# Kernel tuning notes

Measured on AMD Instinct MI355X. Metric: run time of the kernel, lower is better.

## Reference

```python
import jax, jax.numpy as jnp
import numpy as np

D_MODEL = 2048
NUM_HEADS = 16
HEAD_DIM = 128
BATCH = 4
SEQ = 2048


def setup_inputs() -> dict:
    key = jax.random.key(0)
    ks = jax.random.split(key, 5)
    s = 0.02
    return {
        "x": jax.random.normal(ks[0], (BATCH, SEQ, D_MODEL), dtype=jnp.float32),
        "Wq": jax.random.normal(ks[1], (NUM_HEADS * HEAD_DIM, D_MODEL), dtype=jnp.float32) * s,
        "Wk": jax.random.normal(ks[2], (NUM_HEADS * HEAD_DIM, D_MODEL), dtype=jnp.float32) * s,
        "Wv": jax.random.normal(ks[3], (NUM_HEADS * HEAD_DIM, D_MODEL), dtype=jnp.float32) * s,
        "Wo": jax.random.normal(ks[4], (D_MODEL, NUM_HEADS * HEAD_DIM), dtype=jnp.float32) * s,
    }


def _split_heads(t):
    b, s, _ = t.shape
    return t.reshape(b, s, NUM_HEADS, HEAD_DIM).transpose(0, 2, 1, 3)  # [b,h,s,d]


def reference(x, Wq, Wk, Wv, Wo):
    # prefill: QKV proj + causal SDPA + output proj. torch Linear: x @ W.T
    q = _split_heads(x @ Wq.T)
    k = _split_heads(x @ Wk.T)
    v = _split_heads(x @ Wv.T)
    scale = 1.0 / jnp.sqrt(jnp.asarray(HEAD_DIM, dtype=x.dtype))
    scores = jnp.einsum("bhqd,bhkd->bhqk", q, k) * scale
    causal = jnp.tril(jnp.ones((SEQ, SEQ), dtype=bool))
    scores = jnp.where(causal, scores, jnp.finfo(scores.dtype).min)
    attn = jax.nn.softmax(scores, axis=-1)
    y = jnp.einsum("bhqk,bhkd->bhqd", attn, v)
    y = y.transpose(0, 2, 1, 3).reshape(x.shape[0], SEQ, NUM_HEADS * HEAD_DIM)
    y = y @ Wo.T
    return (y, k, v)
```

## Files before the change

kernel.cpp:

```cpp
#include <hip/hip_runtime.h>
#include <stdint.h>

#define DM 2048
#define NH 16
#define HD 128
#define BB 4
#define SS 2048
#define BS (BB*SS)
#define NQKV (3*DM)
#define SCQ 0.12751744565f

typedef __bf16 bf16_t;
typedef __attribute__((ext_vector_type(8))) __bf16 bf16x8;
typedef __attribute__((ext_vector_type(4))) float f32x4;
typedef __attribute__((ext_vector_type(16))) float f32x16;
typedef __attribute__((ext_vector_type(4))) float float4v;
typedef __attribute__((ext_vector_type(4))) unsigned int uint4v;
typedef __attribute__((ext_vector_type(4))) unsigned short ushort4v;
typedef __attribute__((ext_vector_type(8))) unsigned short ushort8;

__device__ __forceinline__ unsigned short f2bf(float f) {
  unsigned u = __float_as_uint(f);
  u += 0x7fffu + ((u >> 16) & 1u);
  return (unsigned short)(u >> 16);
}

__device__ __forceinline__ void gl16(const void* g, void* l) {
  __builtin_amdgcn_global_load_lds(
      (const __attribute__((address_space(1))) unsigned int*)(unsigned long long)g,
      (__attribute__((address_space(3))) unsigned int*)(unsigned int)(unsigned long long)l,
      16, 0, 0);
}

__global__ void conv_f32_bf16(const float* __restrict__ in,
                              unsigned short* __restrict__ out, int n4) {
  int i = blockIdx.x * blockDim.x + threadIdx.x;
  int stride = gridDim.x * blockDim.x;
  for (; i < n4; i += stride) {
    float4v v = ((const float4v*)in)[i];
    ushort4v o;
    o.x = f2bf(v.x); o.y = f2bf(v.y); o.z = f2bf(v.z); o.w = f2bf(v.w);
    ((ushort4v*)out)[i] = o;
  }
}

__global__ void conv_bf16_f32(const unsigned short* __restrict__ in,
                              float* __restrict__ out, int n4) {
  int i = blockIdx.x * blockDim.x + threadIdx.x;
  int stride = gridDim.x * blockDim.x;
  for (; i < n4; i += stride) {
    ushort4v v = ((const ushort4v*)in)[i];
    float4v o;
    o.x = __uint_as_float((unsigned)v.x << 16);
    o.y = __uint_as_float((unsigned)v.y << 16);
    o.z = __uint_as_float((unsigned)v.z << 16);
    o.w = __uint_as_float((unsigned)v.w << 16);
    ((float4v*)out)[i] = o;
  }
}

template<int MODE>
__global__ void gemm_bt(const bf16_t* __restrict__ A, const bf16_t* __restrict__ Bm,
                        const int M, const int N, const int K,
                        float* __restrict__ Cf,
                        bf16_t* __restrict__ qbf,
                        bf16_t* __restrict__ kbt, float* __restrict__ vf) {
  __shared__ bf16_t As[128 * 32];
  __shared__ bf16_t Bs[128 * 32];
  const int t = threadIdx.x;
  const int w = t >> 6, lane = t & 63;
  const int wm = (w >> 1) * 64, wn = (w & 1) * 64;
  const int row0 = blockIdx.x * 128, col0 = blockIdx.y * 128;
  const int fr = lane & 15, fq = lane >> 4;

  f32x4 acc[4][4] = {};

  for (int kk = 0; kk < K; kk += 32) {
#pragma unroll
    for (int j = 0; j < 2; ++j) {
      int idx = j * 256 + t;
      int r = idx >> 2, c = idx & 3;
      uint4v dA = *(const uint4v*)(A + (size_t)(row0 + r) * K + kk + c * 8);
      uint4v dB = *(const uint4v*)(Bm + (size_t)(col0 + r) * K + kk + c * 8);
      int so = r * 32 + ((c ^ (r & 3)) * 8);
      *(uint4v*)(As + so) = dA;
      *(uint4v*)(Bs + so) = dB;
    }
    __syncthreads();
    bf16x8 af[4], bfv[4];
#pragma unroll
    for (int f = 0; f < 4; ++f) {
      int ra = wm + f * 16 + fr;
      af[f] = *(const bf16x8*)(As + ra * 32 + ((fq ^ (ra & 3)) * 8));
      int rb = wn + f * 16 + fr;
      bfv[f] = *(const bf16x8*)(Bs + rb * 32 + ((fq ^ (rb & 3)) * 8));
    }
#pragma unroll
    for (int i = 0; i < 4; ++i)
#pragma unroll
      for (int jn = 0; jn < 4; ++jn)
        acc[i][jn] = __builtin_amdgcn_mfma_f32_16x16x32_bf16(af[i], bfv[jn], acc[i][jn], 0, 0, 0);
    __syncthreads();
  }

#pragma unroll
  for (int i = 0; i < 4; ++i) {
#pragma unroll
    for (int jn = 0; jn < 4; ++jn) {
#pragma unroll
      for (int r = 0; r < 4; ++r) {
        int m = row0 + wm + i * 16 + fq * 4 + r;
        int n = col0 + wn + jn * 16 + fr;
        float v = acc[i][jn][r];
        if (MODE == 0) {
          Cf[(size_t)m * N + n] = v;
        } else {
          int b = m >> 11, s = m & 2047;
          if (n < DM) {
            int h = n >> 7, d = n & 127;
            qbf[(((size_t)(b * NH + h)) * SS + s) * HD + d] = (bf16_t)(v * SCQ);
          } else if (n < 2 * DM) {
            int nn = n - DM, h = nn >> 7, d = nn & 127;
            kbt[(((size_t)(b * NH + h)) * SS + s) * HD + d] = (bf16_t)v;
          } else {
            int nn = n - 2 * DM, h = nn >> 7, d = nn & 127;
            vf[(((size_t)(b * NH + h)) * SS + s) * HD + d] = v;
          }
        }
      }
    }
  }
}

__global__ void vtrans(const float* __restrict__ vf, bf16_t* __restrict__ vt) {
  __shared__ unsigned short T[128 * 64];
  const int t = threadIdx.x;
  const int s0 = blockIdx.x * 64;
  const int bh = blockIdx.y;
  const size_t in_off = (size_t)bh * SS * HD;
  const int sr = t >> 5, c4 = t & 31;
#pragma unroll
  for (int j = 0; j < 8; ++j) {
    int s = j * 8 + sr;
    float4v v = *(const float4v*)(vf + in_off + (size_t)(s0 + s) * HD + c4 * 4);
#pragma unroll
    for (int q = 0; q < 4; ++q) {
      int d = c4 * 4 + q;
      int bc = s * 2;
      int byt = d * 128 + ((((bc >> 4) ^ (d & 7)) << 4) | (bc & 15));
      *(unsigned short*)((char*)T + byt) = f2bf(v[q]);
    }
  }
  __syncthreads();
  const int dr = t >> 3, c8 = t & 7;
  unsigned short* out = (unsigned short*)vt + (size_t)bh * HD * SS;
#pragma unroll
  for (int j = 0; j < 4; ++j) {
    int d = j * 32 + dr;
    ushort8 val = *(const ushort8*)((char*)T + d * 128 + ((c8 ^ (d & 7)) << 4));
    *(ushort8*)(out + (size_t)d * SS + s0 + c8 * 8) = val;
  }
}

__global__ __launch_bounds__(256, 2)
void attn_fwd4(const bf16_t* __restrict__ qbf, const bf16_t* __restrict__ kbf,
               const bf16_t* __restrict__ vt, bf16_t* __restrict__ aout) {
  __shared__ bf16_t Ks[2][64 * 128];
  __shared__ bf16_t Vs[2][64 * 128];
  const int t = threadIdx.x, w = t >> 6, lane = t & 63;
  const int l31 = lane & 31, hi = lane >> 5;
  const int orig = blockIdx.x;
  const int wg = (orig & 7) * 128 + (orig >> 3);
  const int bh = wg >> 4;
  const int qt = 15 - (wg & 15);
  const int q0 = qt * 128;
  const int nt = 2 * qt + 2;
  const size_t bh_off = (size_t)bh * SS * HD;
  const char* kbase = (const char*)(kbf + bh_off);
  const char* vbase = (const char*)(vt + bh_off);

  const char* ksrc[4];
  const char* vsrc[4];
#pragma unroll
  for (int i = 0; i < 4; ++i) {
    int r = (w * 4 + i) * 4 + (lane >> 4);
    int c = (lane & 15) ^ (r & 15);
    ksrc[i] = kbase + r * 256 + c * 16;
    int d = 2 * r + (c >> 3);
    vsrc[i] = vbase + (size_t)d * (SS * 2) + (c & 7) * 16;
  }

  bf16x8 qfr[8];
  {
    const char* qrow = (const char*)(qbf + bh_off + (size_t)(q0 + w * 32 + l31) * HD);
#pragma unroll
    for (int ds = 0; ds < 8; ++ds)
      qfr[ds] = *(const bf16x8*)(qrow + ds * 32 + hi * 16);
  }

#pragma unroll
  for (int i = 0; i < 4; ++i) {
    gl16(ksrc[i], (char*)(&Ks[0][0]) + (w * 4 + i) * 1024);
    gl16(vsrc[i], (char*)(&Vs[0][0]) + (w * 4 + i) * 1024);
    ksrc[i] += 16384;
    vsrc[i] += 128;
  }

  float mrow = -3.0e38f, lrow = 0.f;
  f32x16 accO[4] = {};

  auto make_pa = [&](const f32x16& sv, bf16x8& paA, bf16x8& paB) {
    unsigned W[8];
#pragma unroll
    for (int m = 0; m < 8; ++m) {
      float lo = sv[2 * m], hh = sv[2 * m + 1];
      asm("v_cvt_pk_bf16_f32 %0, %1, %2" : "=v"(W[m]) : "v"(lo), "v"(hh));
    }
#pragma unroll
    for (int g = 0; g < 2; ++g) {
      unsigned A = W[4 * g], B = W[4 * g + 1], C = W[4 * g + 2], D = W[4 * g + 3];
      unsigned xA = (unsigned)__shfl_xor((int)A, 32, 64);
      unsigned xB = (unsigned)__shfl_xor((int)B, 32, 64);
      unsigned xC = (unsigned)__shfl_xor((int)C, 32, 64);
      unsigned xD = (unsigned)__shfl_xor((int)D, 32, 64);
      uint4v u;
      u.x = hi ? xC : A;
      u.y = hi ? xD : B;
      u.z = hi ? C : xA;
      u.w = hi ? D : xB;
      if (g == 0) paA = __builtin_bit_cast(bf16x8, u);
      else        paB = __builtin_bit_cast(bf16x8, u);
    }
  };

  for (int kt = 0; kt < nt; ++kt) {
    const int cur = kt & 1;
    __syncthreads();

    if (kt + 1 < nt) {
#pragma unroll
      for (int i = 0; i < 4; ++i) {
        gl16(ksrc[i], (char*)(&Ks[cur ^ 1][0]) + (w * 4 + i) * 1024);
        gl16(vsrc[i], (char*)(&Vs[cur ^ 1][0]) + (w * 4 + i) * 1024);
        ksrc[i] += 16384;
        vsrc[i] += 128;
      }
    }

    const char* kl = (const char*)&Ks[cur][0];
    f32x16 s0 = {}, s1 = {};
    const int rck = l31 & 15;
    __builtin_amdgcn_s_setprio(1);
#pragma unroll
    for (int ds = 0; ds < 8; ++ds) {
      int ch = ((2 * ds + hi) ^ rck) << 4;
      bf16x8 kf0 = *(const bf16x8*)(kl + l31 * 256 + ch);
      s0 = __builtin_amdgcn_mfma_f32_32x32x16_bf16(kf0, qfr[ds], s0, 0, 0, 0);
      bf16x8 kf1 = *(const bf16x8*)(kl + (32 + l31) * 256 + ch);
      s1 = __builtin_amdgcn_mfma_f32_32x32x16_bf16(kf1, qfr[ds], s1, 0, 0, 0);
    }
    __builtin_amdgcn_s_setprio(0);

    const int kv0 = kt * 64;
    if (kt >= 2 * qt) {
      const int qg = q0 + w * 32 + l31;
#pragma unroll
      for (int r = 0; r < 16; ++r) {
        int klo = kv0 + (r & 3) + 8 * (r >> 2) + 4 * hi;
        if (klo > qg) s0[r] = -3.0e38f;
        if (klo + 32 > qg) s1[r] = -3.0e38f;
      }
    }
    float rm = s0[0];
#pragma unroll
    for (int r = 1; r < 16; ++r) rm = fmaxf(rm, s0[r]);
#pragma unroll
    for (int r = 0; r < 16; ++r) rm = fmaxf(rm, s1[r]);
    rm = fmaxf(rm, __shfl_xor(rm, 32, 64));
    if (__ballot(rm > mrow + 8.0f)) {
      float mnew = fmaxf(mrow, rm);
      float fct = __builtin_amdgcn_exp2f(mrow - mnew);
      mrow = mnew;
      lrow *= fct;
#pragma unroll
      for (int r = 0; r < 16; ++r) {
        float f = __shfl(fct, (r & 3) + 8 * (r >> 2) + 4 * hi, 64);
        accO[0][r] *= f; accO[1][r] *= f; accO[2][r] *= f; accO[3][r] *= f;
      }
    }
    float ss = 0.f;
#pragma unroll
    for (int r = 0; r < 16; ++r) { float p = __builtin_amdgcn_exp2f(s0[r] - mrow); s0[r] = p; ss += p; }
#pragma unroll
    for (int r = 0; r < 16; ++r) { float p = __builtin_amdgcn_exp2f(s1[r] - mrow); s1[r] = p; ss += p; }
    ss += __shfl_xor(ss, 32, 64);
    lrow += ss;

    bf16x8 pa00, pa01, pa10, pa11;
    make_pa(s0, pa00, pa01);
    make_pa(s1, pa10, pa11);

    const char* vl = (const char*)&Vs[cur][0];
    __builtin_amdgcn_s_setprio(1);
#pragma unroll
    for (int dt = 0; dt < 4; ++dt) {
      int R = dt * 16 + (l31 >> 1);
      int cb = (l31 & 1) << 3;
      int rx = R & 15;
      bf16x8 v00 = *(const bf16x8*)(vl + R * 256 + (((cb + 0 + hi) ^ rx) << 4));
      accO[dt] = __builtin_amdgcn_mfma_f32_32x32x16_bf16(pa00, v00, accO[dt], 0, 0, 0);
      bf16x8 v01 = *(const bf16x8*)(vl + R * 256 + (((cb + 2 + hi) ^ rx) << 4));
      accO[dt] = __builtin_amdgcn_mfma_f32_32x32x16_bf16(pa01, v01, accO[dt], 0, 0, 0);
      bf16x8 v10 = *(const bf16x8*)(vl + R * 256 + (((cb + 4 + hi) ^ rx) << 4));
      accO[dt] = __builtin_amdgcn_mfma_f32_32x32x16_bf16(pa10, v10, accO[dt], 0, 0, 0);
      bf16x8 v11 = *(const bf16x8*)(vl + R * 256 + (((cb + 6 + hi) ^ rx) << 4));
      accO[dt] = __builtin_amdgcn_mfma_f32_32x32x16_bf16(pa11, v11, accO[dt], 0, 0, 0);
    }
    __builtin_amdgcn_s_setprio(0);
  }

  const int b = bh >> 4, h = bh & 15;
#pragma unroll
  for (int r = 0; r < 16; ++r) {
    int qr = (r & 3) + 8 * (r >> 2) + 4 * hi;
    float inv = __builtin_amdgcn_rcpf(__shfl(lrow, qr, 64));
    int srow = q0 + w * 32 + qr;
    bf16_t* orow = aout + ((size_t)(b * SS + srow)) * DM + h * HD + l31;
    orow[0]  = (bf16_t)(accO[0][r] * inv);
    orow[32] = (bf16_t)(accO[1][r] * inv);
    orow[64] = (bf16_t)(accO[2][r] * inv);
    orow[96] = (bf16_t)(accO[3][r] * inv);
  }
}

extern "C" void kernel_launch(void* const* d_in, const int* in_sizes, int n_in,
                              void* d_out, int out_size, void* d_ws, size_t ws_size,
                              hipStream_t stream) {
  (void)in_sizes; (void)n_in; (void)out_size; (void)ws_size;
  const float* x  = (const float*)d_in[0];
  const float* Wq = (const float*)d_in[1];
  const float* Wk = (const float*)d_in[2];
  const float* Wv = (const float*)d_in[3];
  const float* Wo = (const float*)d_in[4];

  float* y  = (float*)d_out;
  float* kf = y + (size_t)BS * DM;
  float* vf = kf + (size_t)BS * DM;

  char* ws = (char*)d_ws;
  bf16_t* xbf  = (bf16_t*)ws;
  bf16_t* abf  = xbf;
  bf16_t* qbf  = (bf16_t*)(ws + (size_t)32 * 1024 * 1024);
  bf16_t* wobf = qbf;
  bf16_t* wqkv = (bf16_t*)(ws + (size_t)64 * 1024 * 1024);
  bf16_t* vtb  = wqkv;
  bf16_t* kbt  = (bf16_t*)y;

  conv_f32_bf16<<<2048, 256, 0, stream>>>(x, (unsigned short*)xbf, BS * DM / 4);
  conv_f32_bf16<<<512, 256, 0, stream>>>(Wq, (unsigned short*)wqkv, DM * DM / 4);
  conv_f32_bf16<<<512, 256, 0, stream>>>(Wk, (unsigned short*)(wqkv + (size_t)DM * DM), DM * DM / 4);
  conv_f32_bf16<<<512, 256, 0, stream>>>(Wv, (unsigned short*)(wqkv + 2 * (size_t)DM * DM), DM * DM / 4);

  gemm_bt<1><<<dim3(BS / 128, NQKV / 128), 256, 0, stream>>>(
      xbf, wqkv, BS, NQKV, DM, nullptr, qbf, kbt, vf);

  conv_bf16_f32<<<2048, 256, 0, stream>>>((const unsigned short*)kbt, kf, BS * DM / 4);

  vtrans<<<dim3(SS / 64, BB * NH), 256, 0, stream>>>(vf, vtb);

  attn_fwd4<<<1024, 256, 0, stream>>>(qbf, kbt, vtb, abf);

  conv_f32_bf16<<<512, 256, 0, stream>>>(Wo, (unsigned short*)wobf, DM * DM / 4);

  gemm_bt<0><<<dim3(BS / 128, DM / 128), 256, 0, stream>>>(
      abf, wobf, BS, DM, DM, y, nullptr, nullptr, nullptr);
}
```

Baseline: 531.7 us.

## Replace GEMMs with 256x256 multi-stage async-LDS pipelined kernel and fuse K/V epilogues

Both projection GEMMs move to a new 512-thread kernel with 256x256 tiles. Its four-stage LDS ring is filled by global_load_lds direct copies, with explicit vmcnt waits and raw barriers, and it uses an XCD-aware block remap and MFMA priority boosting. This targets memory latency and low reuse in the old synchronous 128x128 tile GEMM. The QKV epilogue now also writes the fp32 K output and the transposed bf16 V directly, which removes the separate bf16-to-f32 conversion and V-transpose kernels. The cost is strided, scattered epilogue stores for the transposed V and a much larger LDS footprint that limits occupancy.

```diff
diff --git a/kernel.cpp b/kernel.cpp
--- a/kernel.cpp
+++ b/kernel.cpp
@@ -44,74 +44,91 @@
   }
 }
 
-__global__ void conv_bf16_f32(const unsigned short* __restrict__ in,
-                              float* __restrict__ out, int n4) {
-  int i = blockIdx.x * blockDim.x + threadIdx.x;
-  int stride = gridDim.x * blockDim.x;
-  for (; i < n4; i += stride) {
-    ushort4v v = ((const ushort4v*)in)[i];
-    float4v o;
-    o.x = __uint_as_float((unsigned)v.x << 16);
-    o.y = __uint_as_float((unsigned)v.y << 16);
-    o.z = __uint_as_float((unsigned)v.z << 16);
-    o.w = __uint_as_float((unsigned)v.w << 16);
-    ((float4v*)out)[i] = o;
-  }
-}
-
 template<int MODE>
-__global__ void gemm_bt(const bf16_t* __restrict__ A, const bf16_t* __restrict__ Bm,
-                        const int M, const int N, const int K,
-                        float* __restrict__ Cf,
-                        bf16_t* __restrict__ qbf,
-                        bf16_t* __restrict__ kbt, float* __restrict__ vf) {
-  __shared__ bf16_t As[128 * 32];
-  __shared__ bf16_t Bs[128 * 32];
-  const int t = threadIdx.x;
-  const int w = t >> 6, lane = t & 63;
-  const int wm = (w >> 1) * 64, wn = (w & 1) * 64;
-  const int row0 = blockIdx.x * 128, col0 = blockIdx.y * 128;
+__global__ __launch_bounds__(512)
+void gemm256(const bf16_t* __restrict__ A, const bf16_t* __restrict__ Bm,
+             const int K, const int N, const int nbx,
+             float* __restrict__ Cf, bf16_t* __restrict__ qbf,
+             bf16_t* __restrict__ kbt, float* __restrict__ kf,
+             float* __restrict__ vf, bf16_t* __restrict__ vtb) {
+  __shared__ bf16_t As[4][256 * 32];
+  __shared__ bf16_t Bs[4][256 * 32];
+  const int t = threadIdx.x, w = t >> 6, lane = t & 63;
   const int fr = lane & 15, fq = lane >> 4;
-
-  f32x4 acc[4][4] = {};
-
-  for (int kk = 0; kk < K; kk += 32) {
-#pragma unroll
-    for (int j = 0; j < 2; ++j) {
-      int idx = j * 256 + t;
-      int r = idx >> 2, c = idx & 3;
-      uint4v dA = *(const uint4v*)(A + (size_t)(row0 + r) * K + kk + c * 8);
-      uint4v dB = *(const uint4v*)(Bm + (size_t)(col0 + r) * K + kk + c * 8);
-      int so = r * 32 + ((c ^ (r & 3)) * 8);
-      *(uint4v*)(As + so) = dA;
-      *(uint4v*)(Bs + so) = dB;
-    }
-    __syncthreads();
-    bf16x8 af[4], bfv[4];
-#pragma unroll
-    for (int f = 0; f < 4; ++f) {
+  const int cpx = gridDim.x >> 3;
+  const int orig = blockIdx.x;
+  const int wg = (orig & 7) * cpx + (orig >> 3);
+  const int bm = wg % nbx, bn = wg / nbx;
+  const int row0 = bm * 256, col0 = bn * 256;
+  const int wm = (w >> 2) * 128, wn = (w & 3) * 64;
+
+  const int i0 = t, i1 = 512 + t;
+  const int r0 = i0 >> 2, c0 = i0 & 3;
+  const int r1 = i1 >> 2, c1 = i1 & 3;
+  const bf16_t* A0 = A + (size_t)(row0 + r0) * K + ((c0 ^ ((r0 >> 1) & 3)) * 8);
+  const bf16_t* A1 = A + (size_t)(row0 + r1) * K + ((c1 ^ ((r1 >> 1) & 3)) * 8);
+  const bf16_t* B0 = Bm + (size_t)(col0 + r0) * K + ((c0 ^ ((r0 >> 1) & 3)) * 8);
+  const bf16_t* B1 = Bm + (size_t)(col0 + r1) * K + ((c1 ^ ((r1 >> 1) & 3)) * 8);
+
+  const int NT = K >> 5;
+  f32x4 acc[8][4] = {};
+
+#define STAGE(TT)                                                      \
+  {                                                                    \
+    const int sl_ = (TT) & 3;                                          \
+    const size_t ko_ = (size_t)(TT) * 32;                              \
+    gl16(A0 + ko_, (char*)(&As[sl_][0]) + w * 1024);                   \
+    gl16(A1 + ko_, (char*)(&As[sl_][0]) + 8192 + w * 1024);            \
+    gl16(B0 + ko_, (char*)(&Bs[sl_][0]) + w * 1024);                   \
+    gl16(B1 + ko_, (char*)(&Bs[sl_][0]) + 8192 + w * 1024);            \
+  }
+
+  STAGE(0); STAGE(1); STAGE(2);
+
+  for (int T = 0; T < NT; ++T) {
+    if (T + 3 < NT) {
+      STAGE(T + 3);
+      asm volatile("s_waitcnt vmcnt(12)" ::: "memory");
+    } else if (T + 3 == NT) {
+      asm volatile("s_waitcnt vmcnt(8)" ::: "memory");
+    } else if (T + 2 == NT) {
+      asm volatile("s_waitcnt vmcnt(4)" ::: "memory");
+    } else {
+      asm volatile("s_waitcnt vmcnt(0)" ::: "memory");
+    }
+    asm volatile("s_barrier" ::: "memory");
+
+    const bf16_t* al = &As[T & 3][0];
+    const bf16_t* bl = &Bs[T & 3][0];
+    bf16x8 bfv[4];
+#pragma unroll
+    for (int n = 0; n < 4; ++n) {
+      int rb = wn + n * 16 + fr;
+      bfv[n] = *(const bf16x8*)(bl + rb * 32 + ((fq ^ ((rb >> 1) & 3)) * 8));
+    }
+    __builtin_amdgcn_s_setprio(1);
+#pragma unroll
+    for (int f = 0; f < 8; ++f) {
       int ra = wm + f * 16 + fr;
-      af[f] = *(const bf16x8*)(As + ra * 32 + ((fq ^ (ra & 3)) * 8));
-      int rb = wn + f * 16 + fr;
-      bfv[f] = *(const bf16x8*)(Bs + rb * 32 + ((fq ^ (rb & 3)) * 8));
-    }
-#pragma unroll
-    for (int i = 0; i < 4; ++i)
-#pragma unroll
-      for (int jn = 0; jn < 4; ++jn)
-        acc[i][jn] = __builtin_amdgcn_mfma_f32_16x16x32_bf16(af[i], bfv[jn], acc[i][jn], 0, 0, 0);
-    __syncthreads();
-  }
-
-#pragma unroll
-  for (int i = 0; i < 4; ++i) {
+      bf16x8 af = *(const bf16x8*)(al + ra * 32 + ((fq ^ ((ra >> 1) & 3)) * 8));
+#pragma unroll
+      for (int n = 0; n < 4; ++n)
+        acc[f][n] = __builtin_amdgcn_mfma_f32_16x16x32_bf16(af, bfv[n], acc[f][n], 0, 0, 0);
+    }
+    __builtin_amdgcn_s_setprio(0);
+    asm volatile("s_barrier" ::: "memory");
+  }
+#undef STAGE
+
+#pragma unroll
+  for (int f = 0; f < 8; ++f) {
 #pragma unroll
     for (int jn = 0; jn < 4; ++jn) {
 #pragma unroll
       for (int r = 0; r < 4; ++r) {
-        int m = row0 + wm + i * 16 + fq * 4 + r;
+        int m = row0 + wm + f * 16 + fq * 4 + r;
         int n = col0 + wn + jn * 16 + fr;
-        float v = acc[i][jn][r];
+        float v = acc[f][jn][r];
         if (MODE == 0) {
           Cf[(size_t)m * N + n] = v;
         } else {
@@ -121,44 +138,18 @@
             qbf[(((size_t)(b * NH + h)) * SS + s) * HD + d] = (bf16_t)(v * SCQ);
           } else if (n < 2 * DM) {
             int nn = n - DM, h = nn >> 7, d = nn & 127;
-            kbt[(((size_t)(b * NH + h)) * SS + s) * HD + d] = (bf16_t)v;
+            size_t o = (((size_t)(b * NH + h)) * SS + s) * HD + d;
+            kbt[o] = (bf16_t)v;
+            kf[o] = v;
           } else {
             int nn = n - 2 * DM, h = nn >> 7, d = nn & 127;
-            vf[(((size_t)(b * NH + h)) * SS + s) * HD + d] = v;
+            size_t o = (((size_t)(b * NH + h)) * SS + s) * HD + d;
+            vf[o] = v;
+            vtb[((size_t)(b * NH + h)) * (HD * SS) + (size_t)d * SS + s] = (bf16_t)v;
           }
         }
       }
     }
-  }
-}
-
-__global__ void vtrans(const float* __restrict__ vf, bf16_t* __restrict__ vt) {
-  __shared__ unsigned short T[128 * 64];
-  const int t = threadIdx.x;
-  const int s0 = blockIdx.x * 64;
-  const int bh = blockIdx.y;
-  const size_t in_off = (size_t)bh * SS * HD;
-  const int sr = t >> 5, c4 = t & 31;
-#pragma unroll
-  for (int j = 0; j < 8; ++j) {
-    int s = j * 8 + sr;
-    float4v v = *(const float4v*)(vf + in_off + (size_t)(s0 + s) * HD + c4 * 4);
-#pragma unroll
-    for (int q = 0; q < 4; ++q) {
-      int d = c4 * 4 + q;
-      int bc = s * 2;
-      int byt = d * 128 + ((((bc >> 4) ^ (d & 7)) << 4) | (bc & 15));
-      *(unsigned short*)((char*)T + byt) = f2bf(v[q]);
-    }
-  }
-  __syncthreads();
-  const int dr = t >> 3, c8 = t & 7;
-  unsigned short* out = (unsigned short*)vt + (size_t)bh * HD * SS;
-#pragma unroll
-  for (int j = 0; j < 4; ++j) {
-    int d = j * 32 + dr;
-    ushort8 val = *(const ushort8*)((char*)T + d * 128 + ((c8 ^ (d & 7)) << 4));
-    *(ushort8*)(out + (size_t)d * SS + s0 + c8 * 8) = val;
   }
 }
 
@@ -353,25 +344,21 @@
   bf16_t* qbf  = (bf16_t*)(ws + (size_t)32 * 1024 * 1024);
   bf16_t* wobf = qbf;
   bf16_t* wqkv = (bf16_t*)(ws + (size_t)64 * 1024 * 1024);
-  bf16_t* vtb  = wqkv;
   bf16_t* kbt  = (bf16_t*)y;
+  bf16_t* vtb  = (bf16_t*)((char*)y + (size_t)32 * 1024 * 1024);
 
   conv_f32_bf16<<<2048, 256, 0, stream>>>(x, (unsigned short*)xbf, BS * DM / 4);
   conv_f32_bf16<<<512, 256, 0, stream>>>(Wq, (unsigned short*)wqkv, DM * DM / 4);
   conv_f32_bf16<<<512, 256, 0, stream>>>(Wk, (unsigned short*)(wqkv + (size_t)DM * DM), DM * DM / 4);
   conv_f32_bf16<<<512, 256, 0, stream>>>(Wv, (unsigned short*)(wqkv + 2 * (size_t)DM * DM), DM * DM / 4);
 
-  gemm_bt<1><<<dim3(BS / 128, NQKV / 128), 256, 0, stream>>>(
-      xbf, wqkv, BS, NQKV, DM, nullptr, qbf, kbt, vf);
-
-  conv_bf16_f32<<<2048, 256, 0, stream>>>((const unsigned short*)kbt, kf, BS * DM / 4);
-
-  vtrans<<<dim3(SS / 64, BB * NH), 256, 0, stream>>>(vf, vtb);
+  gemm256<1><<<768, 512, 0, stream>>>(
+      xbf, wqkv, DM, NQKV, 32, nullptr, qbf, kbt, kf, vf, vtb);
 
   attn_fwd4<<<1024, 256, 0, stream>>>(qbf, kbt, vtb, abf);
 
   conv_f32_bf16<<<512, 256, 0, stream>>>(Wo, (unsigned short*)wobf, DM * DM / 4);
 
-  gemm_bt<0><<<dim3(BS / 128, DM / 128), 256, 0, stream>>>(
-      abf, wobf, BS, DM, DM, y, nullptr, nullptr, nullptr);
-}
+  gemm256<0><<<256, 512, 0, stream>>>(
+      abf, wobf, DM, DM, 32, y, nullptr, nullptr, nullptr, nullptr, nullptr);
+}
```

After: 529.3 us. No clear change (-0.4%).
